# Kernel optimization log

Measured on AMD Instinct MI355X. Metric: run time of the kernel, lower is better.

## Reference

```python
import jax, jax.numpy as jnp
import numpy as np

D = 128        # node_state_dim
F = 10         # len(CHOSEN_CONNECTION_FEATURES)
N_IP = 20000
N_CONN = 100000
E = 200000
T = 3


def _seg_mean(vals, ids, n):
    s = jax.ops.segment_sum(vals, ids, num_segments=n)
    c = jax.ops.segment_sum(jnp.ones((vals.shape[0], 1), vals.dtype), ids, num_segments=n)
    return s / jnp.maximum(c, 1.0)


def _gru(x, h, kernel, rec_kernel, bias):
    # keras GRUCell, reset_after=True, gate order [z, r, hh]
    xm = x @ kernel + bias[0]
    hm = h @ rec_kernel + bias[1]
    xz, xr, xh = jnp.split(xm, 3, axis=-1)
    hz, hr, hh = jnp.split(hm, 3, axis=-1)
    z = jax.nn.sigmoid(xz + hz)
    r = jax.nn.sigmoid(xr + hr)
    hcand = jnp.tanh(xh + r * hh)
    return z * h + (1.0 - z) * hcand


def setup_inputs() -> dict:
    key = jax.random.key(0)
    ks = jax.random.split(key, 24)
    s = 0.02
    inp = {
        "feature_connection": jax.random.normal(ks[0], (N_CONN, F), jnp.float32),
        "src_ip_to_connection": jax.random.randint(ks[1], (E,), 0, N_IP, jnp.int32),
        "dst_ip_to_connection": jax.random.randint(ks[2], (E,), 0, N_CONN, jnp.int32),
        "src_connection_to_ip": jax.random.randint(ks[3], (E,), 0, N_CONN, jnp.int32),
        "dst_connection_to_ip": jax.random.randint(ks[4], (E,), 0, N_IP, jnp.int32),
        # message MLPs
        "W_m1": jax.random.normal(ks[5], (2 * D, D), jnp.float32) * s,
        "b_m1": jnp.zeros((D,), jnp.float32),
        "W_m2": jax.random.normal(ks[6], (2 * D, D), jnp.float32) * s,
        "b_m2": jnp.zeros((D,), jnp.float32),
        # GRU cells
        "gru_ip_k": jax.random.normal(ks[7], (D, 3 * D), jnp.float32) * s,
        "gru_ip_r": jax.random.normal(ks[8], (D, 3 * D), jnp.float32) * s,
        "gru_ip_b": jnp.zeros((2, 3 * D), jnp.float32),
        "gru_c_k": jax.random.normal(ks[9], (D, 3 * D), jnp.float32) * s,
        "gru_c_r": jax.random.normal(ks[10], (D, 3 * D), jnp.float32) * s,
        "gru_c_b": jnp.zeros((2, 3 * D), jnp.float32),
        # readout MLP
        "W_r1": jax.random.normal(ks[11], (D, 128), jnp.float32) * s,
        "b_r1": jnp.zeros((128,), jnp.float32),
        "W_r2": jax.random.normal(ks[12], (128, 64), jnp.float32) * s,
        "b_r2": jnp.zeros((64,), jnp.float32),
        "W_r3": jax.random.normal(ks[13], (64, 15), jnp.float32) * s,
        "b_r3": jnp.zeros((15,), jnp.float32),
    }
    return inp


def reference(feature_connection, src_ip_to_connection, dst_ip_to_connection,
              src_connection_to_ip, dst_connection_to_ip,
              W_m1, b_m1, W_m2, b_m2,
              gru_ip_k, gru_ip_r, gru_ip_b,
              gru_c_k, gru_c_r, gru_c_b,
              W_r1, b_r1, W_r2, b_r2, W_r3, b_r3):
    ip_state = jnp.ones((N_IP, D), jnp.float32)
    connection_state = jnp.concatenate(
        [feature_connection, jnp.zeros((N_CONN, D - F), jnp.float32)], axis=1)

    for _ in range(T):
        # ip -> connection messages
        nn_in = jnp.concatenate([ip_state[src_ip_to_connection],
                                 connection_state[dst_ip_to_connection]], axis=1)
        ip_message = jax.nn.relu(nn_in @ W_m1 + b_m1)            # [E, D]
        ip_mean = _seg_mean(ip_message, dst_ip_to_connection, N_CONN)
        # connection -> ip messages
        nn_in2 = jnp.concatenate([connection_state[src_connection_to_ip],
                                  ip_state[dst_connection_to_ip]], axis=1)
        conn_message = jax.nn.relu(nn_in2 @ W_m2 + b_m2)         # [E, D]
        conn_mean = _seg_mean(conn_message, dst_connection_to_ip, N_IP)
        # GRU updates
        ip_state = _gru(conn_mean, ip_state, gru_ip_k, gru_ip_r, gru_ip_b)
        connection_state = _gru(ip_mean, connection_state, gru_c_k, gru_c_r, gru_c_b)

    h = jax.nn.relu(connection_state @ W_r1 + b_r1)
    h = jax.nn.relu(h @ W_r2 + b_r2)
    return jax.nn.softmax(h @ W_r3 + b_r3, axis=-1)              # [N_CONN, 15]
```

## Files before the change

kernel.cpp:

```cpp
#include <hip/hip_runtime.h>
#include <math.h>

#define D 128
#define NF 10
#define N_IP 20000
#define N_CONN 100000
#define NE 200000
#define T_ROUNDS 3

typedef unsigned short u16;
using bf16x8 = __attribute__((ext_vector_type(8))) short;
using floatx4 = __attribute__((ext_vector_type(4))) float;

__device__ inline u16 f2bf(float f) {
  union { float f; unsigned u; } v; v.f = f;
  unsigned u = v.u;
  return (u16)((u + 0x7fffu + ((u >> 16) & 1u)) >> 16);
}
__device__ inline float bf2f(u16 h) {
  union { unsigned u; float f; } v; v.u = ((unsigned)h) << 16; return v.f;
}

__device__ inline float fsigmoid(float s) { return 1.f / (1.f + __expf(-s)); }
__device__ inline float ftanh(float a) {
  a = fminf(fmaxf(a, -15.f), 15.f);
  float e = __expf(2.f * a);
  return (e - 1.f) / (e + 1.f);
}

__global__ void k_init_all(u16* __restrict__ ip_state, u16* __restrict__ conn_state,
                           const float* __restrict__ feat, int* __restrict__ cnt) {
  int i = blockIdx.x * blockDim.x + threadIdx.x;
  const int nip = N_IP * D;
  const int nstate = (N_IP + N_CONN) * D;
  if (i < nip) {
    ip_state[i] = 0x3F80;
  } else if (i < nstate) {
    int j = i - nip;
    int r = j >> 7, c = j & 127;
    conn_state[j] = (c < NF) ? f2bf(feat[r * NF + c]) : (u16)0;
  }
  if (i < N_CONN + N_IP) cnt[i] = 0;
}

__global__ void k_prep_all(
    const float* __restrict__ gik, const float* __restrict__ gir,
    const float* __restrict__ gck, const float* __restrict__ gcr,
    const float* __restrict__ Wm1, const float* __restrict__ Wm2,
    const float* __restrict__ Wr1, const float* __restrict__ Wr2,
    u16* __restrict__ gikb, u16* __restrict__ girb,
    u16* __restrict__ gckb, u16* __restrict__ gcrb,
    u16* __restrict__ wm1b, u16* __restrict__ wm2b,
    u16* __restrict__ wm1t, u16* __restrict__ wm2t,
    u16* __restrict__ wr1b, u16* __restrict__ wr2b) {
  int i = blockIdx.x * blockDim.x + threadIdx.x;
  if (i < 196608) {
    int m = i / 49152, r = i % 49152;
    const float* W = (m == 0) ? gik : (m == 1) ? gir : (m == 2) ? gck : gcr;
    u16* Wb = (m == 0) ? gikb : (m == 1) ? girb : (m == 2) ? gckb : gcrb;
    int col = r >> 7, k = r & 127;
    Wb[r] = f2bf(W[k * 384 + col]);
  } else if (i < 278528) {
    int j = i - 196608;
    int m = j / 16384, r = j % 16384;
    const float* W; u16* Wb; int k0;
    if (m == 0) { W = Wm1; Wb = wm1b; k0 = 128; }
    else if (m == 1) { W = Wm2; Wb = wm2b; k0 = 128; }
    else if (m == 2) { W = Wm1; Wb = wm1t; k0 = 0; }
    else if (m == 3) { W = Wm2; Wb = wm2t; k0 = 0; }
    else { W = Wr1; Wb = wr1b; k0 = 0; }
    int col = r >> 7, k = r & 127;
    Wb[r] = f2bf(W[(k0 + k) * 128 + col]);
  } else if (i < 286720) {
    int r = i - 278528;
    int col = r >> 7, k = r & 127;
    wr2b[r] = f2bf(Wr2[k * 64 + col]);
  }
}

__global__ void k_colsum(const float* __restrict__ Wm1, float* __restrict__ csum) {
  int c = threadIdx.x;
  float s = 0.f;
  for (int k = 0; k < 128; k++) s += Wm1[k * 128 + c];
  csum[c] = s;
}

__global__ void k_initP(const float* __restrict__ csum, const float* __restrict__ feat,
                        const float* __restrict__ Wm2,
                        u16* __restrict__ P1, u16* __restrict__ P2) {
  int i = blockIdx.x * blockDim.x + threadIdx.x;
  const int n1 = N_IP * 16;
  const int n2 = N_CONN * 16;
  if (i < n1) {
    int r = i >> 4, g = i & 15;
    u16 v[8];
#pragma unroll
    for (int k = 0; k < 8; k++) v[k] = f2bf(csum[g * 8 + k]);
    *(uint4*)(P1 + (size_t)r * 128 + g * 8) = *(const uint4*)v;
  } else if (i < n1 + n2) {
    int j = i - n1;
    int r = j >> 4, g = j & 15;
    float acc[8] = {0.f, 0.f, 0.f, 0.f, 0.f, 0.f, 0.f, 0.f};
#pragma unroll
    for (int k = 0; k < NF; k++) {
      float f = feat[(size_t)r * NF + k];
      const float* wrow = Wm2 + (size_t)k * 128 + g * 8;
#pragma unroll
      for (int c = 0; c < 8; c++) acc[c] += f * wrow[c];
    }
    u16 v[8];
#pragma unroll
    for (int c = 0; c < 8; c++) v[c] = f2bf(acc[c]);
    *(uint4*)(P2 + (size_t)r * 128 + g * 8) = *(const uint4*)v;
  }
}

__global__ void k_count(const int* __restrict__ d1, const int* __restrict__ d2,
                        int* __restrict__ c1, int* __restrict__ c2) {
  int e = blockIdx.x * blockDim.x + threadIdx.x;
  if (e >= NE) return;
  atomicAdd(&c1[d1[e]], 1);
  atomicAdd(&c2[d2[e]], 1);
}

__global__ void k_scan_part2(const int* __restrict__ cnt1, int* __restrict__ bsum1,
                             int n1, int nb1,
                             const int* __restrict__ cnt2, int* __restrict__ bsum2, int n2) {
  const int* cnt; int* bsum; int n, b;
  if ((int)blockIdx.x < nb1) { cnt = cnt1; bsum = bsum1; n = n1; b = blockIdx.x; }
  else { cnt = cnt2; bsum = bsum2; n = n2; b = blockIdx.x - nb1; }
  int t = threadIdx.x;
  int base = b * 1024 + t * 4;
  int s = 0;
#pragma unroll
  for (int i = 0; i < 4; i++) { int j = base + i; if (j < n) s += cnt[j]; }
  for (int d = 32; d > 0; d >>= 1) s += __shfl_xor(s, d, 64);
  __shared__ int wred[4];
  int lane = t & 63, wv = t >> 6;
  if (lane == 0) wred[wv] = s;
  __syncthreads();
  if (t == 0) bsum[b] = wred[0] + wred[1] + wred[2] + wred[3];
}

__device__ inline void scan_mid_body(int* bsum, int m, int t) {
  int v = (t < m) ? bsum[t] : 0;
  int lane = t & 63, wv = t >> 6;
  int x = v;
  for (int d = 1; d < 64; d <<= 1) { int y = __shfl_up(x, d, 64); if (lane >= d) x += y; }
  __shared__ int wsum[4];
  if (lane == 63) wsum[wv] = x;
  __syncthreads();
  int add = 0;
  for (int i = 0; i < wv; i++) add += wsum[i];
  int ex = add + x - v;
  if (t < m) bsum[t] = ex;
  __syncthreads();
}

__global__ void k_scan_mid2(int* __restrict__ bsum1, int m1, int* __restrict__ bsum2, int m2) {
  int t = threadIdx.x;
  scan_mid_body(bsum1, m1, t);
  scan_mid_body(bsum2, m2, t);
}

__global__ void k_scan_final2(const int* __restrict__ cnt1, const int* __restrict__ bsum1,
                              int* __restrict__ off1, int* __restrict__ cur1, int n1, int nb1,
                              const int* __restrict__ cnt2, const int* __restrict__ bsum2,
                              int* __restrict__ off2, int* __restrict__ cur2, int n2) {
  const int* cnt; const int* bsum; int* off; int* cur; int n, b;
  if ((int)blockIdx.x < nb1) {
    cnt = cnt1; bsum = bsum1; off = off1; cur = cur1; n = n1; b = blockIdx.x;
  } else {
    cnt = cnt2; bsum = bsum2; off = off2; cur = cur2; n = n2; b = blockIdx.x - nb1;
  }
  int t = threadIdx.x;
  int base = b * 1024 + t * 4;
  int vals[4]; int s = 0;
#pragma unroll
  for (int i = 0; i < 4; i++) {
    int j = base + i;
    vals[i] = (j < n) ? cnt[j] : 0;
    s += vals[i];
  }
  int lane = t & 63, wv = t >> 6;
  int x = s;
  for (int d = 1; d < 64; d <<= 1) { int y = __shfl_up(x, d, 64); if (lane >= d) x += y; }
  __shared__ int wsum[4];
  if (lane == 63) wsum[wv] = x;
  __syncthreads();
  int add = 0;
  for (int i = 0; i < wv; i++) add += wsum[i];
  int run = add + x - s + bsum[b];
#pragma unroll
  for (int i = 0; i < 4; i++) {
    int j = base + i;
    if (j < n) { off[j] = run; cur[j] = run; }
    run += vals[i];
  }
}

__global__ void k_scatter(const int* __restrict__ s1, const int* __restrict__ d1,
                          const int* __restrict__ s2, const int* __restrict__ d2,
                          int* __restrict__ cur1, int* __restrict__ cur2,
                          int* __restrict__ o1, int* __restrict__ o2) {
  int e = blockIdx.x * blockDim.x + threadIdx.x;
  if (e >= NE) return;
  int p1 = atomicAdd(&cur1[d1[e]], 1);
  o1[p1] = s1[e];
  int p2 = atomicAdd(&cur2[d2[e]], 1);
  o2[p2] = s2[e];
}

__global__ __launch_bounds__(256, 3) void k_msggru(
    u16* __restrict__ st1, const u16* __restrict__ wq1, const float* __restrict__ qb1,
    const u16* __restrict__ P1g, const int* __restrict__ srcs1g,
    const int* __restrict__ off1g, const int* __restrict__ cnt1g,
    const u16* __restrict__ wx1, const u16* __restrict__ wh1, const float* __restrict__ gb1,
    const u16* __restrict__ wp1, u16* __restrict__ Pn1, int r1, int tiles1,
    u16* __restrict__ st2, const u16* __restrict__ wq2, const float* __restrict__ qb2,
    const u16* __restrict__ P2g, const int* __restrict__ srcs2g,
    const int* __restrict__ off2g, const int* __restrict__ cnt2g,
    const u16* __restrict__ wx2, const u16* __restrict__ wh2, const float* __restrict__ gb2,
    const u16* __restrict__ wp2, u16* __restrict__ Pn2, int r2, int doP) {
  __shared__ __align__(16) char smem[49152];
  __shared__ int offLs[64];
  __shared__ int cntLs[64];
  u16* Wq = (u16*)smem;
  u16* Qb = (u16*)smem;
  u16* Xb = (u16*)(smem + 16384);
  u16* Wg = (u16*)smem;
  u16* Hls = (u16*)(smem + 32768);
  u16* H; const u16* Wqb; const float* qbias; const u16* P;
  const int* srcs; const int* off; const int* cnt;
  const u16* Wxb; const u16* Whb; const float* gbias;
  const u16* Wpt; u16* Pn; int rows, bm;
  if ((int)blockIdx.x < tiles1) {
    H = st1; Wqb = wq1; qbias = qb1; P = P1g; srcs = srcs1g; off = off1g; cnt = cnt1g;
    Wxb = wx1; Whb = wh1; gbias = gb1; Wpt = wp1; Pn = Pn1; rows = r1; bm = blockIdx.x * 64;
  } else {
    H = st2; Wqb = wq2; qbias = qb2; P = P2g; srcs = srcs2g; off = off2g; cnt = cnt2g;
    Wxb = wx2; Whb = wh2; gbias = gb2; Wpt = wp2; Pn = Pn2; rows = r2;
    bm = (blockIdx.x - tiles1) * 64;
  }
  const int tid = threadIdx.x, wv = tid >> 6, lane = tid & 63;
  const int lrow = lane & 15, quad = lane >> 4;
  const uint4 z4 = {0, 0, 0, 0};
#pragma unroll
  for (int i = 0; i < 8; i++) {
    int task = i * 256 + tid;
    int col = task >> 4, gr = task & 15;
    uint4 v = *(const uint4*)(Wqb + (size_t)col * 128 + gr * 8);
    *(uint4*)(Wq + (size_t)col * 128 + ((gr ^ (col & 15)) * 8)) = v;
  }
#pragma unroll
  for (int i = 0; i < 4; i++) {
    int task = i * 256 + tid;
    int row = task >> 4, g = task & 15;
    int grow = bm + row;
    uint4 v = (grow < rows) ? *(const uint4*)(H + (size_t)grow * 128 + g * 8) : z4;
    *(uint4*)(Hls + (size_t)row * 128 + ((g ^ (row & 15)) * 8)) = v;
  }
  if (tid < 64) {
    int node = bm + tid;
    offLs[tid] = (node < rows) ? off[node] : 0;
    cntLs[tid] = (node < rows) ? cnt[node] : 0;
  }
  __syncthreads();
  bf16x8 ah[4];
#pragma unroll
  for (int ks = 0; ks < 4; ks++)
    ah[ks] = *(const bf16x8*)(Hls + (size_t)(wv * 16 + lrow) * 128 + (((ks * 4 + quad) ^ lrow) * 8));
  floatx4 acc[8];
#pragma unroll
  for (int ct = 0; ct < 8; ct++) acc[ct] = {0.f, 0.f, 0.f, 0.f};
#pragma unroll
  for (int ks = 0; ks < 4; ks++) {
#pragma unroll
    for (int ct = 0; ct < 8; ct++) {
      int col = ct * 16 + lrow;
      bf16x8 b = *(const bf16x8*)(Wq + (size_t)col * 128 + (((4 * ks + quad) ^ lrow) * 8));
      acc[ct] = __builtin_amdgcn_mfma_f32_16x16x32_bf16(ah[ks], b, acc[ct], 0, 0, 0);
    }
  }
  __syncthreads();
#pragma unroll
  for (int ct = 0; ct < 8; ct++) {
    int col = ct * 16 + lrow;
    float bv = qbias[col];
#pragma unroll
    for (int reg = 0; reg < 4; reg++) {
      int lr = wv * 16 + quad * 4 + reg;
      Qb[(size_t)lr * 128 + col] = f2bf(acc[ct][reg] + bv);
    }
  }
  __syncthreads();
#pragma unroll
  for (int it = 0; it < 4; it++) {
    int task = it * 256 + tid;
    int nl = task >> 4, g = task & 15;
    int node = bm + nl;
    if (node >= rows) continue;
    int c8 = g << 3;
    float q[8];
    {
      uint4 qv = *(const uint4*)(Qb + (size_t)nl * 128 + c8);
      unsigned qq[4] = {qv.x, qv.y, qv.z, qv.w};
#pragma unroll
      for (int k = 0; k < 4; k++) {
        q[2 * k] = __uint_as_float(qq[k] << 16);
        q[2 * k + 1] = __uint_as_float(qq[k] & 0xffff0000u);
      }
    }
    float acg[8] = {0.f, 0.f, 0.f, 0.f, 0.f, 0.f, 0.f, 0.f};
    int o = offLs[nl], n = cntLs[nl];
    int i = 0;
    for (; i + 4 <= n; i += 4) {
      int s0 = srcs[o + i], s1 = srcs[o + i + 1], s2 = srcs[o + i + 2], s3 = srcs[o + i + 3];
      uint4 v0 = *(const uint4*)(P + (size_t)s0 * 128 + c8);
      uint4 v1 = *(const uint4*)(P + (size_t)s1 * 128 + c8);
      uint4 v2 = *(const uint4*)(P + (size_t)s2 * 128 + c8);
      uint4 v3 = *(const uint4*)(P + (size_t)s3 * 128 + c8);
      unsigned w[16] = {v0.x, v0.y, v0.z, v0.w, v1.x, v1.y, v1.z, v1.w,
                        v2.x, v2.y, v2.z, v2.w, v3.x, v3.y, v3.z, v3.w};
#pragma unroll
      for (int e = 0; e < 4; e++)
#pragma unroll
        for (int k = 0; k < 4; k++) {
          unsigned ww = w[e * 4 + k];
          float lo = __uint_as_float(ww << 16);
          float hi = __uint_as_float(ww & 0xffff0000u);
          acg[2 * k] += fmaxf(lo + q[2 * k], 0.f);
          acg[2 * k + 1] += fmaxf(hi + q[2 * k + 1], 0.f);
        }
    }
    for (; i < n; i++) {
      int s0 = srcs[o + i];
      uint4 v0 = *(const uint4*)(P + (size_t)s0 * 128 + c8);
      unsigned w[4] = {v0.x, v0.y, v0.z, v0.w};
#pragma unroll
      for (int k = 0; k < 4; k++) {
        unsigned ww = w[k];
        float lo = __uint_as_float(ww << 16);
        float hi = __uint_as_float(ww & 0xffff0000u);
        acg[2 * k] += fmaxf(lo + q[2 * k], 0.f);
        acg[2 * k + 1] += fmaxf(hi + q[2 * k + 1], 0.f);
      }
    }
    float inv = 1.f / fmaxf((float)n, 1.f);
    bf16x8 ov;
#pragma unroll
    for (int k = 0; k < 8; k++) ov[k] = (short)f2bf(acg[k] * inv);
    *(bf16x8*)(Xb + (size_t)nl * 128 + ((g ^ (nl & 15)) * 8)) = ov;
  }
  __syncthreads();
  bf16x8 ax[4];
#pragma unroll
  for (int ks = 0; ks < 4; ks++)
    ax[ks] = *(const bf16x8*)(Xb + (size_t)(wv * 16 + lrow) * 128 + (((ks * 4 + quad) ^ lrow) * 8));
  const int lr0 = wv * 16 + quad * 4;
  const u16* gp0; const u16* gp1; const u16* gp2;
  const u16* gp3; const u16* gp4; const u16* gp5;
  u16* lp0; u16* lp1; u16* lp2; u16* lp3; u16* lp4; u16* lp5;
  {
#define MK_PTRS(J, GP, LP)                                                      \
    {                                                                           \
      int task = (J) * 256 + tid;                                               \
      int seg = task >> 8, rem = task & 255;                                    \
      int col = rem >> 4, gr = rem & 15;                                        \
      GP = (seg < 3 ? Wxb : Whb) +                                              \
           (size_t)((seg < 3 ? seg : seg - 3) * 128 + col) * 128 + gr * 8;      \
      LP = Wg + (size_t)(seg * 16 + col) * 128 + ((gr ^ col) * 8);              \
    }
    MK_PTRS(0, gp0, lp0) MK_PTRS(1, gp1, lp1) MK_PTRS(2, gp2, lp2)
    MK_PTRS(3, gp3, lp3) MK_PTRS(4, gp4, lp4) MK_PTRS(5, gp5, lp5)
#undef MK_PTRS
  }
  uint4 v0 = *(const uint4*)(gp0);
  uint4 v1 = *(const uint4*)(gp1);
  uint4 v2 = *(const uint4*)(gp2);
  uint4 v3 = *(const uint4*)(gp3);
  uint4 v4 = *(const uint4*)(gp4);
  uint4 v5 = *(const uint4*)(gp5);
  for (int ch = 0; ch < 8; ch++) {
    __syncthreads();
    *(uint4*)lp0 = v0; *(uint4*)lp1 = v1; *(uint4*)lp2 = v2;
    *(uint4*)lp3 = v3; *(uint4*)lp4 = v4; *(uint4*)lp5 = v5;
    __syncthreads();
    if (ch < 7) {
      size_t d = (size_t)(ch + 1) * 2048;
      v0 = *(const uint4*)(gp0 + d);
      v1 = *(const uint4*)(gp1 + d);
      v2 = *(const uint4*)(gp2 + d);
      v3 = *(const uint4*)(gp3 + d);
      v4 = *(const uint4*)(gp4 + d);
      v5 = *(const uint4*)(gp5 + d);
    }
    floatx4 gacc[3][2];
#pragma unroll
    for (int g = 0; g < 3; g++) {
      gacc[g][0] = {0.f, 0.f, 0.f, 0.f};
      gacc[g][1] = {0.f, 0.f, 0.f, 0.f};
    }
#pragma unroll
    for (int ks = 0; ks < 4; ks++) {
      int posu = ((4 * ks + quad) ^ lrow) * 8;
#pragma unroll
      for (int g = 0; g < 3; g++) {
        bf16x8 bx = *(const bf16x8*)(Wg + (size_t)(g * 16 + lrow) * 128 + posu);
        bf16x8 bh = *(const bf16x8*)(Wg + (size_t)((3 + g) * 16 + lrow) * 128 + posu);
        gacc[g][0] = __builtin_amdgcn_mfma_f32_16x16x32_bf16(ax[ks], bx, gacc[g][0], 0, 0, 0);
        gacc[g][1] = __builtin_amdgcn_mfma_f32_16x16x32_bf16(ah[ks], bh, gacc[g][1], 0, 0, 0);
      }
    }
    int hcol = ch * 16 + lrow;
    float bxz = gbias[hcol];
    float bxr = gbias[128 + hcol];
    float bxh = gbias[256 + hcol];
    float bhz = gbias[384 + hcol];
    float bhr = gbias[384 + 128 + hcol];
    float bhh = gbias[384 + 256 + hcol];
    int ggr = 2 * ch + (lrow >> 3);
    int gel = lrow & 7;
#pragma unroll
    for (int reg = 0; reg < 4; reg++) {
      int lr = lr0 + reg;
      float xz = gacc[0][0][reg] + bxz;
      float xr = gacc[1][0][reg] + bxr;
      float xh = gacc[2][0][reg] + bxh;
      float hz = gacc[0][1][reg] + bhz;
      float hr = gacc[1][1][reg] + bhr;
      float hh = gacc[2][1][reg] + bhh;
      float z = fsigmoid(xz + hz);
      float rr = fsigmoid(xr + hr);
      float hc = ftanh(xh + rr * hh);
      u16* hp = Hls + (size_t)lr * 128 + ((ggr ^ (lr & 15)) * 8) + gel;
      float hold = bf2f(*hp);
      *hp = f2bf(z * hold + (1.f - z) * hc);
    }
  }
  __syncthreads();
#pragma unroll
  for (int i = 0; i < 4; i++) {
    int task = i * 256 + tid;
    int row = task >> 4, g = task & 15;
    int grow = bm + row;
    if (grow < rows)
      *(uint4*)(H + (size_t)grow * 128 + g * 8) =
          *(const uint4*)(Hls + (size_t)row * 128 + ((g ^ (row & 15)) * 8));
  }
  if (!doP) return;
  bf16x8 ah2[4];
#pragma unroll
  for (int ks = 0; ks < 4; ks++)
    ah2[ks] = *(const bf16x8*)(Hls + (size_t)(wv * 16 + lrow) * 128 + (((ks * 4 + quad) ^ lrow) * 8));
  u16* Wp = (u16*)smem;
#pragma unroll
  for (int i = 0; i < 8; i++) {
    int task = i * 256 + tid;
    int col = task >> 4, gr = task & 15;
    uint4 v = *(const uint4*)(Wpt + (size_t)col * 128 + gr * 8);
    *(uint4*)(Wp + (size_t)col * 128 + ((gr ^ (col & 15)) * 8)) = v;
  }
  __syncthreads();
#pragma unroll
  for (int ct = 0; ct < 8; ct++) acc[ct] = {0.f, 0.f, 0.f, 0.f};
#pragma unroll
  for (int ks = 0; ks < 4; ks++) {
#pragma unroll
    for (int ct = 0; ct < 8; ct++) {
      int col = ct * 16 + lrow;
      bf16x8 b = *(const bf16x8*)(Wp + (size_t)col * 128 + (((4 * ks + quad) ^ lrow) * 8));
      acc[ct] = __builtin_amdgcn_mfma_f32_16x16x32_bf16(ah2[ks], b, acc[ct], 0, 0, 0);
    }
  }
  u16* Cls = Hls;
#pragma unroll
  for (int ct = 0; ct < 8; ct++) {
    int col = ct * 16 + lrow;
#pragma unroll
    for (int reg = 0; reg < 4; reg++) {
      int lr = wv * 16 + quad * 4 + reg;
      Cls[(size_t)lr * 128 + col] = f2bf(acc[ct][reg]);
    }
  }
  __syncthreads();
#pragma unroll
  for (int i = 0; i < 4; i++) {
    int task = i * 256 + tid;
    int row = task >> 4, g = task & 15;
    int grow = bm + row;
    if (grow < rows)
      *(uint4*)(Pn + (size_t)grow * 128 + g * 8) =
          *(const uint4*)(Cls + (size_t)row * 128 + g * 8);
  }
}

__global__ __launch_bounds__(256) void k_readout2(
    const u16* __restrict__ S, const u16* __restrict__ W1b, const float* __restrict__ b1,
    const u16* __restrict__ W2b, const float* __restrict__ b2,
    const float* __restrict__ W3, const float* __restrict__ b3,
    float* __restrict__ out, int M) {
  __shared__ __align__(16) char smem[64 * 132 * 4];
  u16* Wls = (u16*)smem;
  u16* H1ls = (u16*)smem;
  u16* W2ls = (u16*)(smem + 17408);
  u16* H2ls = (u16*)smem;
  float* W3ls = (float*)(smem + 9216);
  float* b3ls = (float*)(smem + 9216 + 3840);
  const int tid = threadIdx.x, wv = tid >> 6, lane = tid & 63;
  const int lrow = lane & 15, quad = lane >> 4;
  const int bm = blockIdx.x * 64;
#pragma unroll
  for (int i = 0; i < 8; i++) {
    int task = i * 256 + tid;
    int col = task >> 4, gr = task & 15;
    uint4 v = *(const uint4*)(W1b + (size_t)col * 128 + gr * 8);
    *(uint4*)(Wls + (size_t)col * 128 + ((gr ^ (col & 15)) * 8)) = v;
  }
  const int arow = bm + wv * 16 + lrow;
  const bool arv = arow < M;
  const bf16x8 zv = {0, 0, 0, 0, 0, 0, 0, 0};
  bf16x8 a[4];
#pragma unroll
  for (int ks = 0; ks < 4; ks++)
    a[ks] = arv ? *(const bf16x8*)(S + (size_t)arow * 128 + quad * 8 + ks * 32) : zv;
  __syncthreads();
  floatx4 acc1[8];
#pragma unroll
  for (int ct = 0; ct < 8; ct++) acc1[ct] = {0.f, 0.f, 0.f, 0.f};
#pragma unroll
  for (int ks = 0; ks < 4; ks++) {
#pragma unroll
    for (int ct = 0; ct < 8; ct++) {
      int col = ct * 16 + lrow;
      bf16x8 b = *(const bf16x8*)(Wls + (size_t)col * 128 + (((4 * ks + quad) ^ lrow) * 8));
      acc1[ct] = __builtin_amdgcn_mfma_f32_16x16x32_bf16(a[ks], b, acc1[ct], 0, 0, 0);
    }
  }
  __syncthreads();
#pragma unroll
  for (int ct = 0; ct < 8; ct++) {
    int col = ct * 16 + lrow;
    float bv = b1[col];
#pragma unroll
    for (int reg = 0; reg < 4; reg++) {
      int lr = wv * 16 + quad * 4 + reg;
      H1ls[(size_t)lr * 136 + col] = f2bf(fmaxf(acc1[ct][reg] + bv, 0.f));
    }
  }
#pragma unroll
  for (int i = 0; i < 4; i++) {
    int task = i * 256 + tid;
    int col = task >> 4, gr = task & 15;
    uint4 v = *(const uint4*)(W2b + (size_t)col * 128 + gr * 8);
    *(uint4*)(W2ls + (size_t)col * 128 + ((gr ^ (col & 15)) * 8)) = v;
  }
  __syncthreads();
  bf16x8 a2[4];
#pragma unroll
  for (int ks = 0; ks < 4; ks++)
    a2[ks] = *(const bf16x8*)(H1ls + (size_t)(wv * 16 + lrow) * 136 + quad * 8 + ks * 32);
  floatx4 acc2[4];
#pragma unroll
  for (int ct = 0; ct < 4; ct++) acc2[ct] = {0.f, 0.f, 0.f, 0.f};
#pragma unroll
  for (int ks = 0; ks < 4; ks++) {
#pragma unroll
    for (int ct = 0; ct < 4; ct++) {
      int col = ct * 16 + lrow;
      bf16x8 b = *(const bf16x8*)(W2ls + (size_t)col * 128 + (((4 * ks + quad) ^ lrow) * 8));
      acc2[ct] = __builtin_amdgcn_mfma_f32_16x16x32_bf16(a2[ks], b, acc2[ct], 0, 0, 0);
    }
  }
  __syncthreads();
#pragma unroll
  for (int ct = 0; ct < 4; ct++) {
    int col = ct * 16 + lrow;
    float bv = b2[col];
#pragma unroll
    for (int reg = 0; reg < 4; reg++) {
      int lr = wv * 16 + quad * 4 + reg;
      H2ls[(size_t)lr * 72 + col] = f2bf(fmaxf(acc2[ct][reg] + bv, 0.f));
    }
  }
  for (int l = tid; l < 960; l += 256) W3ls[l] = W3[l];
  if (tid < 15) b3ls[tid] = b3[tid];
  __syncthreads();
  if (tid < 64) {
    int row = tid, gr2 = bm + row;
    if (gr2 < M) {
      float lg[15];
#pragma unroll
      for (int c = 0; c < 15; c++) lg[c] = b3ls[c];
      for (int k = 0; k < 64; k++) {
        float hk = bf2f(H2ls[(size_t)row * 72 + k]);
#pragma unroll
        for (int c = 0; c < 15; c++) lg[c] += hk * W3ls[k * 15 + c];
      }
      float m = lg[0];
#pragma unroll
      for (int c = 1; c < 15; c++) m = fmaxf(m, lg[c]);
      float ssum = 0.f;
#pragma unroll
      for (int c = 0; c < 15; c++) { lg[c] = __expf(lg[c] - m); ssum += lg[c]; }
      float inv = 1.f / ssum;
#pragma unroll
      for (int c = 0; c < 15; c++) out[(size_t)gr2 * 15 + c] = lg[c] * inv;
    }
  }
}

extern "C" void kernel_launch(void* const* d_in, const int* in_sizes, int n_in,
                              void* d_out, int out_size, void* d_ws, size_t ws_size,
                              hipStream_t stream) {
  const float* feat = (const float*)d_in[0];
  const int* src1 = (const int*)d_in[1];
  const int* dst1 = (const int*)d_in[2];
  const int* src2 = (const int*)d_in[3];
  const int* dst2 = (const int*)d_in[4];
  const float* Wm1 = (const float*)d_in[5];
  const float* bm1 = (const float*)d_in[6];
  const float* Wm2 = (const float*)d_in[7];
  const float* bm2 = (const float*)d_in[8];
  const float* gik = (const float*)d_in[9];
  const float* gir = (const float*)d_in[10];
  const float* gib = (const float*)d_in[11];
  const float* gck = (const float*)d_in[12];
  const float* gcr = (const float*)d_in[13];
  const float* gcb = (const float*)d_in[14];
  const float* Wr1 = (const float*)d_in[15];
  const float* br1 = (const float*)d_in[16];
  const float* Wr2 = (const float*)d_in[17];
  const float* br2 = (const float*)d_in[18];
  const float* Wr3 = (const float*)d_in[19];
  const float* br3 = (const float*)d_in[20];
  float* out = (float*)d_out;

  u16* w16 = (u16*)d_ws;
  size_t o = 0;
  u16* ip_state = w16 + o;   o += (size_t)N_IP * D;
  u16* conn_state = w16 + o; o += (size_t)N_CONN * D;
  u16* P1a = w16 + o;        o += (size_t)N_IP * D;
  u16* P2a = w16 + o;        o += (size_t)N_CONN * D;
  u16* P1b = w16 + o;        o += (size_t)N_IP * D;
  u16* P2b = w16 + o;        o += (size_t)N_CONN * D;
  u16* gikb = w16 + o;       o += 49152;
  u16* girb = w16 + o;       o += 49152;
  u16* gckb = w16 + o;       o += 49152;
  u16* gcrb = w16 + o;       o += 49152;
  u16* wm1b = w16 + o;       o += 16384;
  u16* wm2b = w16 + o;       o += 16384;
  u16* wm1t = w16 + o;       o += 16384;
  u16* wm2t = w16 + o;       o += 16384;
  u16* wr1b = w16 + o;       o += 16384;
  u16* wr2b = w16 + o;       o += 8192;
  float* csum = (float*)(w16 + o); o += 256;
  int* ip = (int*)(w16 + o);
  int* cnt1 = ip;  ip += N_CONN;
  int* cnt2 = ip;  ip += N_IP;
  int* off1 = ip;  ip += N_CONN;
  int* off2 = ip;  ip += N_IP;
  int* cur1 = ip;  ip += N_CONN;
  int* cur2 = ip;  ip += N_IP;
  int* srcs1 = ip; ip += NE;
  int* srcs2 = ip; ip += NE;
  int* bsum1 = ip; ip += 256;
  int* bsum2 = ip; ip += 256;

  const int BT = 256;

  const int nstate = (N_IP + N_CONN) * D;
  k_init_all<<<(nstate + BT - 1) / BT, BT, 0, stream>>>(ip_state, conn_state, feat, cnt1);
  k_prep_all<<<(286720 + BT - 1) / BT, BT, 0, stream>>>(
      gik, gir, gck, gcr, Wm1, Wm2, Wr1, Wr2,
      gikb, girb, gckb, gcrb, wm1b, wm2b, wm1t, wm2t, wr1b, wr2b);
  k_colsum<<<1, 128, 0, stream>>>(Wm1, csum);
  const int nPinit = (N_IP + N_CONN) * 16;
  k_initP<<<(nPinit + BT - 1) / BT, BT, 0, stream>>>(csum, feat, Wm2, P1a, P2a);

  k_count<<<(NE + BT - 1) / BT, BT, 0, stream>>>(dst1, dst2, cnt1, cnt2);
  const int nb1 = (N_CONN + 1023) / 1024, nb2 = (N_IP + 1023) / 1024;
  k_scan_part2<<<nb1 + nb2, 256, 0, stream>>>(cnt1, bsum1, N_CONN, nb1, cnt2, bsum2, N_IP);
  k_scan_mid2<<<1, 256, 0, stream>>>(bsum1, nb1, bsum2, nb2);
  k_scan_final2<<<nb1 + nb2, 256, 0, stream>>>(cnt1, bsum1, off1, cur1, N_CONN, nb1,
                                               cnt2, bsum2, off2, cur2, N_IP);
  k_scatter<<<(NE + BT - 1) / BT, BT, 0, stream>>>(src1, dst1, src2, dst2,
                                                   cur1, cur2, srcs1, srcs2);

  const int t64ip = (N_IP + 63) / 64;
  const int t64cn = (N_CONN + 63) / 64;

  u16* P1buf[2] = {P1a, P1b};
  u16* P2buf[2] = {P2a, P2b};
  for (int t = 0; t < T_ROUNDS; t++) {
    int cu = t & 1, nx = cu ^ 1;
    k_msggru<<<t64ip + t64cn, 256, 0, stream>>>(
        ip_state, wm2b, bm2, P2buf[cu], srcs2, off2, cnt2, gikb, girb, gib,
        wm1t, P1buf[nx], N_IP, t64ip,
        conn_state, wm1b, bm1, P1buf[cu], srcs1, off1, cnt1, gckb, gcrb, gcb,
        wm2t, P2buf[nx], N_CONN, (t < T_ROUNDS - 1) ? 1 : 0);
  }

  k_readout2<<<t64cn, 256, 0, stream>>>(conn_state, wr1b, br1, wr2b, br2,
                                        Wr3, br3, out, N_CONN);
}
```

Before: 493.3 us.

## Use async global-to-LDS loads, shrink LDS, fuse setup kernels, parallelize readout softmax

Merges the column-sum into the weight prep kernel and the edge counting into the P init kernel to cut launches. In the message/GRU kernel, the per-block staging of weight matrices into LDS is dropped: dense weights are read straight from global (cache) and GRU weights are streamed with global_load_lds into two buffers. This shrinks LDS so occupancy can rise to 4 blocks. The readout softmax is spread over 16 lanes per row with shuffle reductions instead of one thread per row. Risks include uncached global weight fetches per MFMA and unguarded loads of rows beyond the tensor end.

```diff
diff --git a/kernel.cpp b/kernel.cpp
--- a/kernel.cpp
+++ b/kernel.cpp
@@ -26,6 +26,12 @@
   a = fminf(fmaxf(a, -15.f), 15.f);
   float e = __expf(2.f * a);
   return (e - 1.f) / (e + 1.f);
+}
+
+__device__ __forceinline__ void gld16(const u16* g, u16* l) {
+  __builtin_amdgcn_global_load_lds(
+      (const __attribute__((address_space(1))) unsigned int*)g,
+      (__attribute__((address_space(3))) unsigned int*)l, 16, 0, 0);
 }
 
 __global__ void k_init_all(u16* __restrict__ ip_state, u16* __restrict__ conn_state,
@@ -52,7 +58,7 @@
     u16* __restrict__ gckb, u16* __restrict__ gcrb,
     u16* __restrict__ wm1b, u16* __restrict__ wm2b,
     u16* __restrict__ wm1t, u16* __restrict__ wm2t,
-    u16* __restrict__ wr1b, u16* __restrict__ wr2b) {
+    u16* __restrict__ wr1b, u16* __restrict__ wr2b, float* __restrict__ csum) {
   int i = blockIdx.x * blockDim.x + threadIdx.x;
   if (i < 196608) {
     int m = i / 49152, r = i % 49152;
@@ -75,20 +81,24 @@
     int r = i - 278528;
     int col = r >> 7, k = r & 127;
     wr2b[r] = f2bf(Wr2[k * 64 + col]);
-  }
-}
-
-__global__ void k_colsum(const float* __restrict__ Wm1, float* __restrict__ csum) {
-  int c = threadIdx.x;
-  float s = 0.f;
-  for (int k = 0; k < 128; k++) s += Wm1[k * 128 + c];
-  csum[c] = s;
-}
-
-__global__ void k_initP(const float* __restrict__ csum, const float* __restrict__ feat,
-                        const float* __restrict__ Wm2,
-                        u16* __restrict__ P1, u16* __restrict__ P2) {
+  } else if (i < 286848) {
+    int c = i - 286720;
+    float s = 0.f;
+    for (int k = 0; k < 128; k++) s += Wm1[k * 128 + c];
+    csum[c] = s;
+  }
+}
+
+__global__ void k_initP_count(const float* __restrict__ csum, const float* __restrict__ feat,
+                              const float* __restrict__ Wm2,
+                              u16* __restrict__ P1, u16* __restrict__ P2,
+                              const int* __restrict__ d1, const int* __restrict__ d2,
+                              int* __restrict__ c1, int* __restrict__ c2) {
   int i = blockIdx.x * blockDim.x + threadIdx.x;
+  if (i < NE) {
+    atomicAdd(&c1[d1[i]], 1);
+    atomicAdd(&c2[d2[i]], 1);
+  }
   const int n1 = N_IP * 16;
   const int n2 = N_CONN * 16;
   if (i < n1) {
@@ -113,14 +123,6 @@
     for (int c = 0; c < 8; c++) v[c] = f2bf(acc[c]);
     *(uint4*)(P2 + (size_t)r * 128 + g * 8) = *(const uint4*)v;
   }
-}
-
-__global__ void k_count(const int* __restrict__ d1, const int* __restrict__ d2,
-                        int* __restrict__ c1, int* __restrict__ c2) {
-  int e = blockIdx.x * blockDim.x + threadIdx.x;
-  if (e >= NE) return;
-  atomicAdd(&c1[d1[e]], 1);
-  atomicAdd(&c2[d2[e]], 1);
 }
 
 __global__ void k_scan_part2(const int* __restrict__ cnt1, int* __restrict__ bsum1,
@@ -211,7 +213,7 @@
   o2[p2] = s2[e];
 }
 
-__global__ __launch_bounds__(256, 3) void k_msggru(
+__global__ __launch_bounds__(256, 4) void k_msggru(
     u16* __restrict__ st1, const u16* __restrict__ wq1, const float* __restrict__ qb1,
     const u16* __restrict__ P1g, const int* __restrict__ srcs1g,
     const int* __restrict__ off1g, const int* __restrict__ cnt1g,
@@ -222,14 +224,13 @@
     const int* __restrict__ off2g, const int* __restrict__ cnt2g,
     const u16* __restrict__ wx2, const u16* __restrict__ wh2, const float* __restrict__ gb2,
     const u16* __restrict__ wp2, u16* __restrict__ Pn2, int r2, int doP) {
-  __shared__ __align__(16) char smem[49152];
-  __shared__ int offLs[64];
-  __shared__ int cntLs[64];
-  u16* Wq = (u16*)smem;
+  __shared__ __align__(16) char smem[40960];
   u16* Qb = (u16*)smem;
-  u16* Xb = (u16*)(smem + 16384);
-  u16* Wg = (u16*)smem;
-  u16* Hls = (u16*)(smem + 32768);
+  u16* bufA = (u16*)smem;
+  u16* bufB = (u16*)(smem + 12288);
+  u16* Hls = (u16*)(smem + 24576);
+  int* offLs = (int*)(smem + 24064);
+  int* cntLs = (int*)(smem + 24320);
   u16* H; const u16* Wqb; const float* qbias; const u16* P;
   const int* srcs; const int* off; const int* cnt;
   const u16* Wxb; const u16* Whb; const float* gbias;
@@ -244,21 +245,12 @@
   }
   const int tid = threadIdx.x, wv = tid >> 6, lane = tid & 63;
   const int lrow = lane & 15, quad = lane >> 4;
-  const uint4 z4 = {0, 0, 0, 0};
-#pragma unroll
-  for (int i = 0; i < 8; i++) {
-    int task = i * 256 + tid;
-    int col = task >> 4, gr = task & 15;
-    uint4 v = *(const uint4*)(Wqb + (size_t)col * 128 + gr * 8);
-    *(uint4*)(Wq + (size_t)col * 128 + ((gr ^ (col & 15)) * 8)) = v;
-  }
+  const int c4 = lane >> 4, slot = lane & 15;
+  const int rowl = wv * 4 + c4;
 #pragma unroll
   for (int i = 0; i < 4; i++) {
-    int task = i * 256 + tid;
-    int row = task >> 4, g = task & 15;
-    int grow = bm + row;
-    uint4 v = (grow < rows) ? *(const uint4*)(H + (size_t)grow * 128 + g * 8) : z4;
-    *(uint4*)(Hls + (size_t)row * 128 + ((g ^ (row & 15)) * 8)) = v;
+    gld16(H + (size_t)(bm + i * 16 + rowl) * 128 + ((slot ^ rowl) * 8),
+          Hls + (size_t)(i * 16 + wv * 4) * 128 + lane * 8);
   }
   if (tid < 64) {
     int node = bm + tid;
@@ -277,12 +269,10 @@
   for (int ks = 0; ks < 4; ks++) {
 #pragma unroll
     for (int ct = 0; ct < 8; ct++) {
-      int col = ct * 16 + lrow;
-      bf16x8 b = *(const bf16x8*)(Wq + (size_t)col * 128 + (((4 * ks + quad) ^ lrow) * 8));
+      bf16x8 b = *(const bf16x8*)(Wqb + (size_t)(ct * 16 + lrow) * 128 + (4 * ks + quad) * 8);
       acc[ct] = __builtin_amdgcn_mfma_f32_16x16x32_bf16(ah[ks], b, acc[ct], 0, 0, 0);
     }
   }
-  __syncthreads();
 #pragma unroll
   for (int ct = 0; ct < 8; ct++) {
     int col = ct * 16 + lrow;
@@ -350,51 +340,25 @@
     bf16x8 ov;
 #pragma unroll
     for (int k = 0; k < 8; k++) ov[k] = (short)f2bf(acg[k] * inv);
-    *(bf16x8*)(Xb + (size_t)nl * 128 + ((g ^ (nl & 15)) * 8)) = ov;
+    *(bf16x8*)(Qb + (size_t)nl * 128 + ((g ^ (nl & 15)) * 8)) = ov;
   }
   __syncthreads();
   bf16x8 ax[4];
 #pragma unroll
   for (int ks = 0; ks < 4; ks++)
-    ax[ks] = *(const bf16x8*)(Xb + (size_t)(wv * 16 + lrow) * 128 + (((ks * 4 + quad) ^ lrow) * 8));
+    ax[ks] = *(const bf16x8*)(Qb + (size_t)(wv * 16 + lrow) * 128 + (((ks * 4 + quad) ^ lrow) * 8));
   const int lr0 = wv * 16 + quad * 4;
-  const u16* gp0; const u16* gp1; const u16* gp2;
-  const u16* gp3; const u16* gp4; const u16* gp5;
-  u16* lp0; u16* lp1; u16* lp2; u16* lp3; u16* lp4; u16* lp5;
-  {
-#define MK_PTRS(J, GP, LP)                                                      \
-    {                                                                           \
-      int task = (J) * 256 + tid;                                               \
-      int seg = task >> 8, rem = task & 255;                                    \
-      int col = rem >> 4, gr = rem & 15;                                        \
-      GP = (seg < 3 ? Wxb : Whb) +                                              \
-           (size_t)((seg < 3 ? seg : seg - 3) * 128 + col) * 128 + gr * 8;      \
-      LP = Wg + (size_t)(seg * 16 + col) * 128 + ((gr ^ col) * 8);              \
-    }
-    MK_PTRS(0, gp0, lp0) MK_PTRS(1, gp1, lp1) MK_PTRS(2, gp2, lp2)
-    MK_PTRS(3, gp3, lp3) MK_PTRS(4, gp4, lp4) MK_PTRS(5, gp5, lp5)
-#undef MK_PTRS
-  }
-  uint4 v0 = *(const uint4*)(gp0);
-  uint4 v1 = *(const uint4*)(gp1);
-  uint4 v2 = *(const uint4*)(gp2);
-  uint4 v3 = *(const uint4*)(gp3);
-  uint4 v4 = *(const uint4*)(gp4);
-  uint4 v5 = *(const uint4*)(gp5);
+  __syncthreads();
+#pragma unroll
+  for (int j = 0; j < 3; j++)
+    gld16(Wxb + (size_t)(j * 128 + 0 * 16 + rowl) * 128 + ((slot ^ rowl) * 8),
+          bufA + (size_t)(j * 16 + wv * 4) * 128 + lane * 8);
   for (int ch = 0; ch < 8; ch++) {
     __syncthreads();
-    *(uint4*)lp0 = v0; *(uint4*)lp1 = v1; *(uint4*)lp2 = v2;
-    *(uint4*)lp3 = v3; *(uint4*)lp4 = v4; *(uint4*)lp5 = v5;
-    __syncthreads();
-    if (ch < 7) {
-      size_t d = (size_t)(ch + 1) * 2048;
-      v0 = *(const uint4*)(gp0 + d);
-      v1 = *(const uint4*)(gp1 + d);
-      v2 = *(const uint4*)(gp2 + d);
-      v3 = *(const uint4*)(gp3 + d);
-      v4 = *(const uint4*)(gp4 + d);
-      v5 = *(const uint4*)(gp5 + d);
-    }
+#pragma unroll
+    for (int j = 0; j < 3; j++)
+      gld16(Whb + (size_t)(j * 128 + ch * 16 + rowl) * 128 + ((slot ^ rowl) * 8),
+            bufB + (size_t)(j * 16 + wv * 4) * 128 + lane * 8);
     floatx4 gacc[3][2];
 #pragma unroll
     for (int g = 0; g < 3; g++) {
@@ -406,9 +370,23 @@
       int posu = ((4 * ks + quad) ^ lrow) * 8;
 #pragma unroll
       for (int g = 0; g < 3; g++) {
-        bf16x8 bx = *(const bf16x8*)(Wg + (size_t)(g * 16 + lrow) * 128 + posu);
-        bf16x8 bh = *(const bf16x8*)(Wg + (size_t)((3 + g) * 16 + lrow) * 128 + posu);
+        bf16x8 bx = *(const bf16x8*)(bufA + (size_t)(g * 16 + lrow) * 128 + posu);
         gacc[g][0] = __builtin_amdgcn_mfma_f32_16x16x32_bf16(ax[ks], bx, gacc[g][0], 0, 0, 0);
+      }
+    }
+    __syncthreads();
+    if (ch < 7) {
+#pragma unroll
+      for (int j = 0; j < 3; j++)
+        gld16(Wxb + (size_t)(j * 128 + (ch + 1) * 16 + rowl) * 128 + ((slot ^ rowl) * 8),
+              bufA + (size_t)(j * 16 + wv * 4) * 128 + lane * 8);
+    }
+#pragma unroll
+    for (int ks = 0; ks < 4; ks++) {
+      int posu = ((4 * ks + quad) ^ lrow) * 8;
+#pragma unroll
+      for (int g = 0; g < 3; g++) {
+        bf16x8 bh = *(const bf16x8*)(bufB + (size_t)(g * 16 + lrow) * 128 + posu);
         gacc[g][1] = __builtin_amdgcn_mfma_f32_16x16x32_bf16(ah[ks], bh, gacc[g][1], 0, 0, 0);
       }
     }
@@ -453,26 +431,17 @@
 #pragma unroll
   for (int ks = 0; ks < 4; ks++)
     ah2[ks] = *(const bf16x8*)(Hls + (size_t)(wv * 16 + lrow) * 128 + (((ks * 4 + quad) ^ lrow) * 8));
-  u16* Wp = (u16*)smem;
-#pragma unroll
-  for (int i = 0; i < 8; i++) {
-    int task = i * 256 + tid;
-    int col = task >> 4, gr = task & 15;
-    uint4 v = *(const uint4*)(Wpt + (size_t)col * 128 + gr * 8);
-    *(uint4*)(Wp + (size_t)col * 128 + ((gr ^ (col & 15)) * 8)) = v;
-  }
-  __syncthreads();
 #pragma unroll
   for (int ct = 0; ct < 8; ct++) acc[ct] = {0.f, 0.f, 0.f, 0.f};
 #pragma unroll
   for (int ks = 0; ks < 4; ks++) {
 #pragma unroll
     for (int ct = 0; ct < 8; ct++) {
-      int col = ct * 16 + lrow;
-      bf16x8 b = *(const bf16x8*)(Wp + (size_t)col * 128 + (((4 * ks + quad) ^ lrow) * 8));
+      bf16x8 b = *(const bf16x8*)(Wpt + (size_t)(ct * 16 + lrow) * 128 + (4 * ks + quad) * 8);
       acc[ct] = __builtin_amdgcn_mfma_f32_16x16x32_bf16(ah2[ks], b, acc[ct], 0, 0, 0);
     }
   }
+  __syncthreads();
   u16* Cls = Hls;
 #pragma unroll
   for (int ct = 0; ct < 8; ct++) {
@@ -495,28 +464,19 @@
   }
 }
 
-__global__ __launch_bounds__(256) void k_readout2(
+__global__ __launch_bounds__(256, 4) void k_readout2(
     const u16* __restrict__ S, const u16* __restrict__ W1b, const float* __restrict__ b1,
     const u16* __restrict__ W2b, const float* __restrict__ b2,
     const float* __restrict__ W3, const float* __restrict__ b3,
     float* __restrict__ out, int M) {
-  __shared__ __align__(16) char smem[64 * 132 * 4];
-  u16* Wls = (u16*)smem;
+  __shared__ __align__(16) char smem[17408];
   u16* H1ls = (u16*)smem;
-  u16* W2ls = (u16*)(smem + 17408);
   u16* H2ls = (u16*)smem;
   float* W3ls = (float*)(smem + 9216);
   float* b3ls = (float*)(smem + 9216 + 3840);
   const int tid = threadIdx.x, wv = tid >> 6, lane = tid & 63;
   const int lrow = lane & 15, quad = lane >> 4;
   const int bm = blockIdx.x * 64;
-#pragma unroll
-  for (int i = 0; i < 8; i++) {
-    int task = i * 256 + tid;
-    int col = task >> 4, gr = task & 15;
-    uint4 v = *(const uint4*)(W1b + (size_t)col * 128 + gr * 8);
-    *(uint4*)(Wls + (size_t)col * 128 + ((gr ^ (col & 15)) * 8)) = v;
-  }
   const int arow = bm + wv * 16 + lrow;
   const bool arv = arow < M;
   const bf16x8 zv = {0, 0, 0, 0, 0, 0, 0, 0};
@@ -524,7 +484,6 @@
 #pragma unroll
   for (int ks = 0; ks < 4; ks++)
     a[ks] = arv ? *(const bf16x8*)(S + (size_t)arow * 128 + quad * 8 + ks * 32) : zv;
-  __syncthreads();
   floatx4 acc1[8];
 #pragma unroll
   for (int ct = 0; ct < 8; ct++) acc1[ct] = {0.f, 0.f, 0.f, 0.f};
@@ -532,12 +491,10 @@
   for (int ks = 0; ks < 4; ks++) {
 #pragma unroll
     for (int ct = 0; ct < 8; ct++) {
-      int col = ct * 16 + lrow;
-      bf16x8 b = *(const bf16x8*)(Wls + (size_t)col * 128 + (((4 * ks + quad) ^ lrow) * 8));
+      bf16x8 b = *(const bf16x8*)(W1b + (size_t)(ct * 16 + lrow) * 128 + (4 * ks + quad) * 8);
       acc1[ct] = __builtin_amdgcn_mfma_f32_16x16x32_bf16(a[ks], b, acc1[ct], 0, 0, 0);
     }
   }
-  __syncthreads();
 #pragma unroll
   for (int ct = 0; ct < 8; ct++) {
     int col = ct * 16 + lrow;
@@ -548,13 +505,6 @@
       H1ls[(size_t)lr * 136 + col] = f2bf(fmaxf(acc1[ct][reg] + bv, 0.f));
     }
   }
-#pragma unroll
-  for (int i = 0; i < 4; i++) {
-    int task = i * 256 + tid;
-    int col = task >> 4, gr = task & 15;
-    uint4 v = *(const uint4*)(W2b + (size_t)col * 128 + gr * 8);
-    *(uint4*)(W2ls + (size_t)col * 128 + ((gr ^ (col & 15)) * 8)) = v;
-  }
   __syncthreads();
   bf16x8 a2[4];
 #pragma unroll
@@ -567,8 +517,7 @@
   for (int ks = 0; ks < 4; ks++) {
 #pragma unroll
     for (int ct = 0; ct < 4; ct++) {
-      int col = ct * 16 + lrow;
-      bf16x8 b = *(const bf16x8*)(W2ls + (size_t)col * 128 + (((4 * ks + quad) ^ lrow) * 8));
+      bf16x8 b = *(const bf16x8*)(W2b + (size_t)(ct * 16 + lrow) * 128 + (4 * ks + quad) * 8);
       acc2[ct] = __builtin_amdgcn_mfma_f32_16x16x32_bf16(a2[ks], b, acc2[ct], 0, 0, 0);
     }
   }
@@ -586,26 +535,32 @@
   for (int l = tid; l < 960; l += 256) W3ls[l] = W3[l];
   if (tid < 15) b3ls[tid] = b3[tid];
   __syncthreads();
-  if (tid < 64) {
-    int row = tid, gr2 = bm + row;
-    if (gr2 < M) {
-      float lg[15];
-#pragma unroll
-      for (int c = 0; c < 15; c++) lg[c] = b3ls[c];
+  {
+    int col = tid & 15;
+    int rb = (tid >> 4) * 4;
+    float lg[4] = {0.f, 0.f, 0.f, 0.f};
+    if (col < 15) {
+      float b3v = b3ls[col];
+      lg[0] = b3v; lg[1] = b3v; lg[2] = b3v; lg[3] = b3v;
       for (int k = 0; k < 64; k++) {
-        float hk = bf2f(H2ls[(size_t)row * 72 + k]);
-#pragma unroll
-        for (int c = 0; c < 15; c++) lg[c] += hk * W3ls[k * 15 + c];
+        float w = W3ls[k * 15 + col];
+#pragma unroll
+        for (int r = 0; r < 4; r++)
+          lg[r] += bf2f(H2ls[(size_t)(rb + r) * 72 + k]) * w;
       }
-      float m = lg[0];
-#pragma unroll
-      for (int c = 1; c < 15; c++) m = fmaxf(m, lg[c]);
-      float ssum = 0.f;
-#pragma unroll
-      for (int c = 0; c < 15; c++) { lg[c] = __expf(lg[c] - m); ssum += lg[c]; }
-      float inv = 1.f / ssum;
-#pragma unroll
-      for (int c = 0; c < 15; c++) out[(size_t)gr2 * 15 + c] = lg[c] * inv;
+    }
+#pragma unroll
+    for (int r = 0; r < 4; r++) {
+      float v = (col < 15) ? lg[r] : -3.0e38f;
+      float m = v;
+#pragma unroll
+      for (int d = 1; d < 16; d <<= 1) m = fmaxf(m, __shfl_xor(m, d, 16));
+      float e = (col < 15) ? __expf(lg[r] - m) : 0.f;
+      float s = e;
+#pragma unroll
+      for (int d = 1; d < 16; d <<= 1) s += __shfl_xor(s, d, 16);
+      int gr2 = bm + rb + r;
+      if (col < 15 && gr2 < M) out[(size_t)gr2 * 15 + col] = e / s;
     }
   }
 }
@@ -671,14 +626,13 @@
 
   const int nstate = (N_IP + N_CONN) * D;
   k_init_all<<<(nstate + BT - 1) / BT, BT, 0, stream>>>(ip_state, conn_state, feat, cnt1);
-  k_prep_all<<<(286720 + BT - 1) / BT, BT, 0, stream>>>(
+  k_prep_all<<<(286848 + BT - 1) / BT, BT, 0, stream>>>(
       gik, gir, gck, gcr, Wm1, Wm2, Wr1, Wr2,
-      gikb, girb, gckb, gcrb, wm1b, wm2b, wm1t, wm2t, wr1b, wr2b);
-  k_colsum<<<1, 128, 0, stream>>>(Wm1, csum);
+      gikb, girb, gckb, gcrb, wm1b, wm2b, wm1t, wm2t, wr1b, wr2b, csum);
   const int nPinit = (N_IP + N_CONN) * 16;
-  k_initP<<<(nPinit + BT - 1) / BT, BT, 0, stream>>>(csum, feat, Wm2, P1a, P2a);
-
-  k_count<<<(NE + BT - 1) / BT, BT, 0, stream>>>(dst1, dst2, cnt1, cnt2);
+  k_initP_count<<<(nPinit + BT - 1) / BT, BT, 0, stream>>>(
+      csum, feat, Wm2, P1a, P2a, dst1, dst2, cnt1, cnt2);
+
   const int nb1 = (N_CONN + 1023) / 1024, nb2 = (N_IP + 1023) / 1024;
   k_scan_part2<<<nb1 + nb2, 256, 0, stream>>>(cnt1, bsum1, N_CONN, nb1, cnt2, bsum2, N_IP);
   k_scan_mid2<<<1, 256, 0, stream>>>(bsum1, nb1, bsum2, nb2);
```

Result: slower. 567.7 us (+15.1%).
